# Performance work log

Measured on AMD Instinct MI355X. Metric: run time of the kernel, lower is better.

## Reference

```python
import jax, jax.numpy as jnp
import numpy as np

NP_, NA, NPR = 3000, 25, 1071
N = NP_ + NA + NPR          # 4096 total nodes
D = 256                     # latent_dim
H = 8                       # num_heads
DH = D // H                 # head dim 32
FF = 4 * D                  # feed-forward dim
BLOCKS = 3                  # args.block_num
E = 131072                  # edges = N * 32 avg degree
EPS = 1e-5


def setup_inputs() -> dict:
    key = jax.random.key(0)
    ks = jax.random.split(key, 16)
    s = 1.0 / np.sqrt(D)
    return {
        "adj_row": jax.random.randint(ks[0], (E,), 0, N, dtype=jnp.int32),
        "adj_col": jax.random.randint(ks[1], (E,), 0, N, dtype=jnp.int32),
        "adj_val": jax.random.uniform(ks[2], (E,), dtype=jnp.float32),
        "pe": jax.random.normal(ks[3], (NP_, D), dtype=jnp.float32) * s,
        "ae": jax.random.normal(ks[4], (NA, D), dtype=jnp.float32) * s,
        "qe": jax.random.normal(ks[5], (NPR, D), dtype=jnp.float32) * s,
        "Wqkv": jax.random.normal(ks[6], (D, 3 * D), dtype=jnp.float32) * s,
        "Wo": jax.random.normal(ks[7], (D, D), dtype=jnp.float32) * s,
        "W1": jax.random.normal(ks[8], (D, FF), dtype=jnp.float32) * s,
        "b1": jnp.zeros((FF,), dtype=jnp.float32),
        "W2": jax.random.normal(ks[9], (FF, D), dtype=jnp.float32) * (1.0 / np.sqrt(FF)),
        "b2": jnp.zeros((D,), dtype=jnp.float32),
        "ln1_g": jnp.ones((D,), dtype=jnp.float32),
        "ln1_b": jnp.zeros((D,), dtype=jnp.float32),
        "ln2_g": jnp.ones((D,), dtype=jnp.float32),
        "ln2_b": jnp.zeros((D,), dtype=jnp.float32),
    }


def _layer_norm(x, g, b):
    m = jnp.mean(x, axis=-1, keepdims=True)
    v = jnp.mean(jnp.square(x - m), axis=-1, keepdims=True)
    return (x - m) * jax.lax.rsqrt(v + EPS) * g + b


def _encoder_layer(x, Wqkv, Wo, W1, b1, W2, b2, ln1_g, ln1_b, ln2_g, ln2_b):
    # x: [N, D]; standard post-LN transformer encoder (dropout = 0)
    qkv = x @ Wqkv                                   # [N, 3D]
    q, k, v = jnp.split(qkv, 3, axis=-1)
    q = q.reshape(N, H, DH)
    k = k.reshape(N, H, DH)
    v = v.reshape(N, H, DH)
    scores = jnp.einsum("nhd,mhd->hnm", q, k) / np.sqrt(DH)  # [H, N, N]
    att = jax.nn.softmax(scores, axis=-1)
    o = jnp.einsum("hnm,mhd->nhd", att, v).reshape(N, D) @ Wo
    x = _layer_norm(x + o, ln1_g, ln1_b)
    h = jax.nn.relu(x @ W1 + b1) @ W2 + b2
    return _layer_norm(x + h, ln2_g, ln2_b)


def _spmm(adj_row, adj_col, adj_val, x):
    # sparse [N,N] @ dense [N,D] via gather + segment-sum scatter
    msgs = adj_val[:, None] * x[adj_col]             # [E, D]
    return jax.ops.segment_sum(msgs, adj_row, num_segments=N)


def reference(adj_row, adj_col, adj_val, pe, ae, qe, Wqkv, Wo, W1, b1, W2, b2,
              ln1_g, ln1_b, ln2_g, ln2_b):
    cur = jnp.concatenate([pe, ae, qe], axis=0)      # [N, D]
    total = cur
    for _ in range(BLOCKS):
        t = _spmm(adj_row, adj_col, adj_val, cur)
        t = _encoder_layer(t, Wqkv, Wo, W1, b1, W2, b2, ln1_g, ln1_b, ln2_g, ln2_b)
        cur = t + cur                                # residual per block
        total = total + cur                          # sum over embeds list
    protein = total[:NP_]
    aa = total[NP_:NP_ + NA]
    prop = total[NP_ + NA:]
    return total, protein, aa, prop
```

## Files before the change

### kernel.cpp

```cpp
#include <hip/hip_runtime.h>
#include <hip/hip_bf16.h>


#define NPROT 3000
#define NAA   25
#define NPROP 1071
#define NTOT  4096
#define DIM   256
#define NH    8
#define DHD   32
#define FFD   1024
#define NEDGE 131072
#define LNEPS 1e-5f
#define KSPLIT 2
#define KVQ (NTOT/KSPLIT)

typedef unsigned short u16;
typedef unsigned int u32;
typedef __attribute__((ext_vector_type(8))) short short8v;
typedef __attribute__((ext_vector_type(4))) float float4v;
typedef __attribute__((ext_vector_type(2))) unsigned int uint2v;

__device__ __forceinline__ u16 f2bu(float x){
  union { __hip_bfloat16 h; u16 u; } c; c.h = __float2bfloat16(x); return c.u;
}
__device__ __forceinline__ float bu2f(u16 u){
  union { u32 i; float f; } c; c.i = ((u32)u) << 16; return c.f;
}
__device__ __forceinline__ float4v mfma16(short8v a, short8v b, float4v c){
  return __builtin_amdgcn_mfma_f32_16x16x32_bf16(a, b, c, 0, 0, 0);
}
__device__ __forceinline__ u32 packbf(float lo, float hi){
  u32 ul = __builtin_bit_cast(u32, lo);
  u32 uh = __builtin_bit_cast(u32, hi);
  return (ul >> 16) | (uh & 0xFFFF0000u);
}

__global__ __launch_bounds__(256) void k_embed(const float* __restrict__ pe, const float* __restrict__ ae,
                                               const float* __restrict__ qe,
                                               float* __restrict__ cur, float* __restrict__ tot){
  int i = blockIdx.x*256 + threadIdx.x;
  int row = i >> 8;
  float v;
  if (row < NPROT)           v = pe[i];
  else if (row < NPROT+NAA)  v = ae[i - NPROT*DIM];
  else                       v = qe[i - (NPROT+NAA)*DIM];
  cur[i] = v; tot[i] = v;
}

__global__ __launch_bounds__(256) void k_zero(int* __restrict__ p, int n){
  int i = blockIdx.x*256 + threadIdx.x; if (i < n) p[i] = 0;
}

__global__ __launch_bounds__(256) void k_wconv_all(const float* __restrict__ Wqkv, const float* __restrict__ Wo,
                                                   const float* __restrict__ W1, const float* __restrict__ W2,
                                                   u16* __restrict__ wqkvt, u16* __restrict__ wot,
                                                   u16* __restrict__ w1t, u16* __restrict__ w2t){
  int b = blockIdx.x;
  const float* W; u16* Wt; int K, N, n;
  if (b < 768)       { W = Wqkv; Wt = wqkvt; K = 256;  N = 768;  n = b; }
  else if (b < 1024) { W = Wo;   Wt = wot;   K = 256;  N = 256;  n = b - 768; }
  else if (b < 2048) { W = W1;   Wt = w1t;   K = 256;  N = 1024; n = b - 1024; }
  else               { W = W2;   Wt = w2t;   K = 1024; N = 256;  n = b - 2048; }
  for (int k = threadIdx.x; k < K; k += 256)
    Wt[(size_t)n*K + k] = f2bu(W[(size_t)k*N + n]);
}

__global__ __launch_bounds__(256) void k_hist(const int* __restrict__ rows, int* __restrict__ cnt){
  int e = blockIdx.x*256 + threadIdx.x; if (e < NEDGE) atomicAdd(&cnt[rows[e]], 1);
}

__global__ __launch_bounds__(64) void k_scan(const int* __restrict__ cnt, int* __restrict__ rowptr,
                                             int* __restrict__ cursor){
  int lane = threadIdx.x;
  int sum = 0;
  for (int i = 0; i < 64; ++i) sum += cnt[lane*64 + i];
  int pref = sum;
  #pragma unroll
  for (int off = 1; off < 64; off <<= 1){
    int u = __shfl_up(pref, off);
    if (lane >= off) pref += u;
  }
  int run = pref - sum;
  for (int i = 0; i < 64; ++i){
    int c = cnt[lane*64 + i];
    rowptr[lane*64 + i] = run;
    cursor[lane*64 + i] = run;
    run += c;
  }
  if (lane == 63) rowptr[NTOT] = run;
}

__global__ __launch_bounds__(256) void k_scatter(const int* __restrict__ rows, const int* __restrict__ cols,
                                                 const float* __restrict__ vals, int* __restrict__ cursor,
                                                 int* __restrict__ ccol, float* __restrict__ cval){
  int e = blockIdx.x*256 + threadIdx.x; if (e >= NEDGE) return;
  int p = atomicAdd(&cursor[rows[e]], 1);
  ccol[p] = cols[e]; cval[p] = vals[e];
}

__global__ __launch_bounds__(256) void k_spmm(const int* __restrict__ rowptr, const int* __restrict__ ccol,
                                              const float* __restrict__ cval, const float* __restrict__ x,
                                              float* __restrict__ out, u16* __restrict__ outb){
  int r = blockIdx.x, c = threadIdx.x;
  int s = rowptr[r], e = rowptr[r+1];
  float acc = 0.f;
  for (int i = s; i < e; ++i)
    acc += cval[i] * x[((size_t)ccol[i] << 8) + c];
  out[((size_t)r << 8) + c] = acc;
  outb[((size_t)r << 8) + c] = f2bu(acc);
}

template<int RELU, int BIAS, int BF16OUT>
__global__ __launch_bounds__(256) void k_gemm64(const u16* __restrict__ A, const u16* __restrict__ Wt,
                                                const float* __restrict__ bias, void* __restrict__ Cv,
                                                int M, int K, int Nc){
  __shared__ u16 Al[64*64];
  __shared__ u16 Bl[64*64];
  const int tid = threadIdx.x;
  const int w  = tid >> 6, l = tid & 63, lr = l & 15, g = l >> 4;
  const int row0 = blockIdx.y*64, col0 = blockIdx.x*64;
  const int wm = (w >> 1)*32, wn = (w & 1)*32;
  const int sm = tid >> 2;
  const int so = (tid & 3)*2;
  float4v acc[2][2] = {};

  for (int k0 = 0; k0 < K; k0 += 64){
    const u16* As = A  + (size_t)(row0 + sm)*K + k0 + so*8;
    const u16* Bs = Wt + (size_t)(col0 + sm)*K + k0 + so*8;
    #pragma unroll
    for (int j = 0; j < 2; ++j){
      int o = so + j;
      int slot = o ^ (sm & 7);
      *(short8v*)(Al + sm*64 + slot*8) = *(const short8v*)(As + j*8);
      *(short8v*)(Bl + sm*64 + slot*8) = *(const short8v*)(Bs + j*8);
    }
    __syncthreads();
    #pragma unroll
    for (int kk = 0; kk < 2; ++kk){
      short8v af[2], bfr[2];
      #pragma unroll
      for (int i = 0; i < 2; ++i){
        int am = wm + 16*i + lr;
        af[i]  = *(const short8v*)(Al + am*64 + (((4*kk + g) ^ (am & 7))*8));
        int bn = wn + 16*i + lr;
        bfr[i] = *(const short8v*)(Bl + bn*64 + (((4*kk + g) ^ (bn & 7))*8));
      }
      acc[0][0] = mfma16(af[0], bfr[0], acc[0][0]);
      acc[0][1] = mfma16(af[0], bfr[1], acc[0][1]);
      acc[1][0] = mfma16(af[1], bfr[0], acc[1][0]);
      acc[1][1] = mfma16(af[1], bfr[1], acc[1][1]);
    }
    __syncthreads();
  }

  #pragma unroll
  for (int mi = 0; mi < 2; ++mi){
    #pragma unroll
    for (int ni = 0; ni < 2; ++ni){
      int col = col0 + wn + 16*ni + lr;
      float bv = BIAS ? bias[col] : 0.f;
      #pragma unroll
      for (int j = 0; j < 4; ++j){
        int row = row0 + wm + 16*mi + 4*g + j;
        float v = acc[mi][ni][j] + bv;
        if (RELU) v = fmaxf(v, 0.f);
        if (BF16OUT) ((u16*)Cv)[(size_t)row*Nc + col] = f2bu(v);
        else         ((float*)Cv)[(size_t)row*Nc + col] = v;
      }
    }
  }
}

__global__ __launch_bounds__(256) void k_attn_mfma(const u16* __restrict__ qbf,
                                                   u16* __restrict__ op,
                                                   float* __restrict__ mbuf, float* __restrict__ lbuf){
  __shared__ u16 Vt[2][32*64];
  __shared__ u16 Pl[4][16*64];
  __shared__ float Fl[4][16];
  const int h   = blockIdx.y;
  const int ks  = blockIdx.z;
  const int qb  = blockIdx.x * 64;
  const int tid = threadIdx.x;
  const int w   = tid >> 6;
  const int l   = tid & 63;
  const int lr  = l & 15;
  const int g   = l >> 4;
  const int sr  = tid >> 2;
  const int sq  = tid & 3;
  const float SC  = 0.17677669529663687f;
  const float SCL = 0.25503837f;
  const float DEFER = 31.368f;
  u16* opart = op + (size_t)ks*NTOT*DIM;

  short8v qf = *(const short8v*)(qbf + (size_t)(qb + 16*w + lr)*768 + h*DHD + 8*g);
  short8v ones;
  #pragma unroll
  for (int j = 0; j < 8; ++j) ones[j] = (short)0x3F80;

  float4v oa0 = {0.f,0.f,0.f,0.f}, oa1 = {0.f,0.f,0.f,0.f};
  float4v accl = {0.f,0.f,0.f,0.f};
  float mrun = -1e30f;
  u16* pw = &Pl[w][0];

  const u16* vp = qbf + (size_t)(ks*KVQ + sr)*768 + 512 + h*DHD + 8*sq;
  const u16* kp = qbf + (size_t)(ks*KVQ + lr)*768 + 256 + h*DHD + 8*g;
  short8v vreg = *(const short8v*)vp;
  short8v kf0 = *(const short8v*)(kp);
  short8v kf1 = *(const short8v*)(kp + (size_t)16*768);
  short8v kf2 = *(const short8v*)(kp + (size_t)32*768);
  short8v kf3 = *(const short8v*)(kp + (size_t)48*768);

  const int NIT = KVQ/64;
  for (int t = 0; t < NIT; ++t){
    u16* vt = &Vt[t & 1][0];
    #pragma unroll
    for (int j = 0; j < 8; ++j){
      int row  = 8*sq + j;
      int slot = (sr >> 3) ^ j;
      vt[row*64 + slot*8 + (sr & 7)] = (u16)vreg[j];
    }
    __syncthreads();
    vp += (size_t)64*768;
    if (t + 1 < NIT) vreg = *(const short8v*)vp;

    float4v s0 = mfma16(kf0, qf, (float4v){0.f,0.f,0.f,0.f});
    float4v s1 = mfma16(kf1, qf, (float4v){0.f,0.f,0.f,0.f});
    float4v s2 = mfma16(kf2, qf, (float4v){0.f,0.f,0.f,0.f});
    float4v s3 = mfma16(kf3, qf, (float4v){0.f,0.f,0.f,0.f});
    if (t + 1 < NIT){
      const u16* kn = kp + (size_t)(t+1)*64*768;
      kf0 = *(const short8v*)(kn);
      kf1 = *(const short8v*)(kn + (size_t)16*768);
      kf2 = *(const short8v*)(kn + (size_t)32*768);
      kf3 = *(const short8v*)(kn + (size_t)48*768);
    }

    float m0 = fmaxf(fmaxf(fmaxf(s0[0],s0[1]),s0[2]),s0[3]);
    float m1 = fmaxf(fmaxf(fmaxf(s1[0],s1[1]),s1[2]),s1[3]);
    float m2 = fmaxf(fmaxf(fmaxf(s2[0],s2[1]),s2[2]),s2[3]);
    float m3 = fmaxf(fmaxf(fmaxf(s3[0],s3[1]),s3[2]),s3[3]);
    float tm = fmaxf(fmaxf(fmaxf(m0,m1),m2),m3);
    tm = fmaxf(tm, __shfl_xor(tm, 16));
    tm = fmaxf(tm, __shfl_xor(tm, 32));
    const bool nomax = __all(tm <= mrun + DEFER);
    float fac = 1.f;
    if (!nomax){
      float mn = fmaxf(mrun, tm);
      fac = exp2f((mrun - mn)*SCL);
      mrun = mn;
    }
    float mns = mrun*SCL;
    #pragma unroll
    for (int j = 0; j < 4; ++j){
      s0[j] = exp2f(__builtin_fmaf(s0[j], SCL, -mns));
      s1[j] = exp2f(__builtin_fmaf(s1[j], SCL, -mns));
      s2[j] = exp2f(__builtin_fmaf(s2[j], SCL, -mns));
      s3[j] = exp2f(__builtin_fmaf(s3[j], SCL, -mns));
    }

    {
      int gh = g >> 1, gl = 4*(g & 1);
      uint2v* d0 = (uint2v*)(pw + lr*64 + ((0 + gh) ^ (lr & 7))*8 + gl);
      uint2v* d1 = (uint2v*)(pw + lr*64 + ((2 + gh) ^ (lr & 7))*8 + gl);
      uint2v* d2 = (uint2v*)(pw + lr*64 + ((4 + gh) ^ (lr & 7))*8 + gl);
      uint2v* d3 = (uint2v*)(pw + lr*64 + ((6 + gh) ^ (lr & 7))*8 + gl);
      *d0 = (uint2v){packbf(s0[0],s0[1]), packbf(s0[2],s0[3])};
      *d1 = (uint2v){packbf(s1[0],s1[1]), packbf(s1[2],s1[3])};
      *d2 = (uint2v){packbf(s2[0],s2[1]), packbf(s2[2],s2[3])};
      *d3 = (uint2v){packbf(s3[0],s3[1]), packbf(s3[2],s3[3])};
    }

    if (!nomax){
      if (g == 0) Fl[w][lr] = fac;
      float fq0 = Fl[w][4*g+0], fq1 = Fl[w][4*g+1], fq2 = Fl[w][4*g+2], fq3 = Fl[w][4*g+3];
      oa0[0]*=fq0; oa0[1]*=fq1; oa0[2]*=fq2; oa0[3]*=fq3;
      oa1[0]*=fq0; oa1[1]*=fq1; oa1[2]*=fq2; oa1[3]*=fq3;
      accl[0]*=fq0; accl[1]*=fq1; accl[2]*=fq2; accl[3]*=fq3;
    }

    #pragma unroll
    for (int kk = 0; kk < 2; ++kk){
      int slotp = (4*kk + g) ^ (lr & 7);
      short8v pa = *(const short8v*)(pw + lr*64 + slotp*8);
      short8v v0 = *(const short8v*)(vt + lr*64        + slotp*8);
      short8v v1 = *(const short8v*)(vt + (lr+16)*64   + slotp*8);
      oa0  = mfma16(pa, v0, oa0);
      oa1  = mfma16(pa, v1, oa1);
      accl = mfma16(pa, ones, accl);
    }
  }

  #pragma unroll
  for (int j = 0; j < 4; ++j){
    size_t row = (size_t)(qb + 16*w + 4*g + j);
    opart[row*DIM + h*DHD + lr]      = f2bu(oa0[j]);
    opart[row*DIM + h*DHD + 16 + lr] = f2bu(oa1[j]);
  }
  if (l < 16){
    size_t mi = (size_t)(ks*NH + h)*NTOT + qb + 16*w + lr;
    mbuf[mi] = mrun*SC;
  }
  if (lr == 0){
    #pragma unroll
    for (int j = 0; j < 4; ++j){
      size_t mi = (size_t)(ks*NH + h)*NTOT + qb + 16*w + 4*g + j;
      lbuf[mi] = accl[j];
    }
  }
}

__global__ __launch_bounds__(256) void k_attn_merge(const u16* __restrict__ op,
                                                    const float* __restrict__ mbuf, const float* __restrict__ lbuf,
                                                    u16* __restrict__ obf){
  int i = blockIdx.x*256 + threadIdx.x;
  int r = i >> 8, c = i & 255, h = c >> 5;
  float m[KSPLIT], wgt[KSPLIT];
  float M = -1e30f;
  #pragma unroll
  for (int k = 0; k < KSPLIT; ++k){
    m[k] = mbuf[(size_t)(k*NH + h)*NTOT + r];
    M = fmaxf(M, m[k]);
  }
  float L = 0.f, acc = 0.f;
  #pragma unroll
  for (int k = 0; k < KSPLIT; ++k){
    wgt[k] = __expf(m[k] - M);
    L   += wgt[k]*lbuf[(size_t)(k*NH + h)*NTOT + r];
    acc += wgt[k]*bu2f(op[(size_t)k*NTOT*DIM + i]);
  }
  obf[i] = f2bu(acc / L);
}

template<int DUAL>
__global__ __launch_bounds__(256) void k_add_ln(const float* __restrict__ a, const float* __restrict__ b,
                                                const float* __restrict__ g, const float* __restrict__ be,
                                                float* __restrict__ out, u16* __restrict__ out2){
  __shared__ float red[4];
  int r = blockIdx.x, c = threadIdx.x;
  float v = a[((size_t)r << 8) + c] + b[((size_t)r << 8) + c];
  float s = v;
  #pragma unroll
  for (int off = 32; off; off >>= 1) s += __shfl_down(s, off);
  if ((c & 63) == 0) red[c >> 6] = s;
  __syncthreads();
  float mean = (red[0]+red[1]+red[2]+red[3]) * (1.f/DIM);
  __syncthreads();
  float d = v - mean;
  float s2 = d*d;
  #pragma unroll
  for (int off = 32; off; off >>= 1) s2 += __shfl_down(s2, off);
  if ((c & 63) == 0) red[c >> 6] = s2;
  __syncthreads();
  float var = (red[0]+red[1]+red[2]+red[3]) * (1.f/DIM);
  float rv = d * rsqrtf(var + LNEPS) * g[c] + be[c];
  out[((size_t)r << 8) + c] = rv;
  if (DUAL) out2[((size_t)r << 8) + c] = f2bu(rv);
}

template<int FINAL>
__global__ __launch_bounds__(256) void k_add_ln_upd(const float* __restrict__ a, const float* __restrict__ b,
                                                    const float* __restrict__ g, const float* __restrict__ be,
                                                    float* __restrict__ cur, float* __restrict__ tot,
                                                    float* __restrict__ out){
  __shared__ float red[4];
  int r = blockIdx.x, c = threadIdx.x;
  size_t idx = ((size_t)r << 8) + c;
  float v = a[idx] + b[idx];
  float s = v;
  #pragma unroll
  for (int off = 32; off; off >>= 1) s += __shfl_down(s, off);
  if ((c & 63) == 0) red[c >> 6] = s;
  __syncthreads();
  float mean = (red[0]+red[1]+red[2]+red[3]) * (1.f/DIM);
  __syncthreads();
  float d = v - mean;
  float s2 = d*d;
  #pragma unroll
  for (int off = 32; off; off >>= 1) s2 += __shfl_down(s2, off);
  if ((c & 63) == 0) red[c >> 6] = s2;
  __syncthreads();
  float var = (red[0]+red[1]+red[2]+red[3]) * (1.f/DIM);
  float rv = d * rsqrtf(var + LNEPS) * g[c] + be[c];
  float cu = cur[idx] + rv;
  cur[idx] = cu;
  float tv = tot[idx] + cu;
  tot[idx] = tv;
  if (FINAL){
    out[idx] = tv;
    out[(size_t)NTOT*DIM + idx] = tv;
  }
}

extern "C" void kernel_launch(void* const* d_in, const int* in_sizes, int n_in,
                              void* d_out, int out_size, void* d_ws, size_t ws_size,
                              hipStream_t stream){
  const int*   adj_row = (const int*)  d_in[0];
  const int*   adj_col = (const int*)  d_in[1];
  const float* adj_val = (const float*)d_in[2];
  const float* pe   = (const float*)d_in[3];
  const float* ae   = (const float*)d_in[4];
  const float* qe   = (const float*)d_in[5];
  const float* Wqkv = (const float*)d_in[6];
  const float* Wo   = (const float*)d_in[7];
  const float* W1   = (const float*)d_in[8];
  const float* b1   = (const float*)d_in[9];
  const float* W2   = (const float*)d_in[10];
  const float* b2   = (const float*)d_in[11];
  const float* g1   = (const float*)d_in[12];
  const float* be1  = (const float*)d_in[13];
  const float* g2   = (const float*)d_in[14];
  const float* be2  = (const float*)d_in[15];
  float* out = (float*)d_out;

  char* w = (char*)d_ws;
  float* cur  = (float*)w; w += (size_t)NTOT*DIM*4;
  float* tot  = (float*)w; w += (size_t)NTOT*DIM*4;
  float* tf   = (float*)w; w += (size_t)NTOT*DIM*4;
  float* pbuf = (float*)w; w += (size_t)NTOT*DIM*4;
  float* x1   = (float*)w; w += (size_t)NTOT*DIM*4;
  u16* tbf    = (u16*)w;   w += (size_t)NTOT*DIM*2;
  u16* obf    = (u16*)w;   w += (size_t)NTOT*DIM*2;
  u16* x1b    = (u16*)w;   w += (size_t)NTOT*DIM*2;
  u16* hq     = (u16*)w;   w += (size_t)NTOT*FFD*2;
  u16* wqkvt  = (u16*)w;   w += (size_t)768*256*2;
  u16* wot    = (u16*)w;   w += (size_t)256*256*2;
  u16* w1t    = (u16*)w;   w += (size_t)1024*256*2;
  u16* w2t    = (u16*)w;   w += (size_t)256*1024*2;
  int* rowptr = (int*)w;   w += (size_t)(NTOT+1)*4;
  int* cnt    = (int*)w;   w += (size_t)NTOT*4;
  int* cursor = (int*)w;   w += (size_t)NTOT*4;
  int* ccol   = (int*)w;   w += (size_t)NEDGE*4;
  float* cval = (float*)w; w += (size_t)NEDGE*4;
  u16* qbf  = hq;
  u16* opbf = (u16*)pbuf;
  float* mbuf = (float*)tbf;
  float* lbuf = mbuf + (size_t)KSPLIT*NH*NTOT;

  k_zero<<<16, 256, 0, stream>>>(cnt, NTOT);
  k_embed<<<NTOT, 256, 0, stream>>>(pe, ae, qe, cur, tot);
  k_hist<<<NEDGE/256, 256, 0, stream>>>(adj_row, cnt);
  k_scan<<<1, 64, 0, stream>>>(cnt, rowptr, cursor);
  k_scatter<<<NEDGE/256, 256, 0, stream>>>(adj_row, adj_col, adj_val, cursor, ccol, cval);
  k_wconv_all<<<2304, 256, 0, stream>>>(Wqkv, Wo, W1, W2, wqkvt, wot, w1t, w2t);

  for (int blk = 0; blk < 3; ++blk){
    k_spmm<<<NTOT, 256, 0, stream>>>(rowptr, ccol, cval, cur, tf, tbf);
    k_gemm64<0,0,1><<<dim3(768/64, NTOT/64), 256, 0, stream>>>(tbf, wqkvt, nullptr, qbf, NTOT, 256, 768);
    k_attn_mfma<<<dim3(NTOT/64, NH, KSPLIT), 256, 0, stream>>>(qbf, opbf, mbuf, lbuf);
    k_attn_merge<<<NTOT*DIM/256, 256, 0, stream>>>(opbf, mbuf, lbuf, obf);
    k_gemm64<0,0,0><<<dim3(256/64, NTOT/64), 256, 0, stream>>>(obf, wot, nullptr, pbuf, NTOT, 256, 256);
    k_add_ln<1><<<NTOT, 256, 0, stream>>>(tf, pbuf, g1, be1, x1, x1b);
    k_gemm64<1,1,1><<<dim3(1024/64, NTOT/64), 256, 0, stream>>>(x1b, w1t, b1, hq, NTOT, 256, 1024);
    k_gemm64<0,1,0><<<dim3(256/64, NTOT/64), 256, 0, stream>>>(hq, w2t, b2, pbuf, NTOT, 1024, 256);
    if (blk < 2)
      k_add_ln_upd<0><<<NTOT, 256, 0, stream>>>(x1, pbuf, g2, be2, cur, tot, nullptr);
    else
      k_add_ln_upd<1><<<NTOT, 256, 0, stream>>>(x1, pbuf, g2, be2, cur, tot, out);
  }
}
```

Measured before the change: 476.1 us.

## Write V transposed from QKV GEMM and drop LDS V transpose in attention

```diff
diff --git a/kernel.cpp b/kernel.cpp
--- a/kernel.cpp
+++ b/kernel.cpp
@@ -111,9 +111,10 @@
   outb[((size_t)r << 8) + c] = f2bu(acc);
 }
 
-template<int RELU, int BIAS, int BF16OUT>
+template<int RELU, int BIAS, int BF16OUT, int VSPLIT>
 __global__ __launch_bounds__(256) void k_gemm64(const u16* __restrict__ A, const u16* __restrict__ Wt,
                                                 const float* __restrict__ bias, void* __restrict__ Cv,
+                                                u16* __restrict__ vtg,
                                                 int M, int K, int Nc){
   __shared__ u16 Al[64*64];
   __shared__ u16 Bl[64*64];
@@ -158,26 +159,33 @@
   for (int mi = 0; mi < 2; ++mi){
     #pragma unroll
     for (int ni = 0; ni < 2; ++ni){
-      int col = col0 + wn + 16*ni + lr;
-      float bv = BIAS ? bias[col] : 0.f;
-      #pragma unroll
-      for (int j = 0; j < 4; ++j){
-        int row = row0 + wm + 16*mi + 4*g + j;
-        float v = acc[mi][ni][j] + bv;
-        if (RELU) v = fmaxf(v, 0.f);
-        if (BF16OUT) ((u16*)Cv)[(size_t)row*Nc + col] = f2bu(v);
-        else         ((float*)Cv)[(size_t)row*Nc + col] = v;
+      int colbase = col0 + wn + 16*ni;
+      int col = colbase + lr;
+      if (VSPLIT && colbase >= 512){
+        int row = row0 + wm + 16*mi + 4*g;
+        u32 lo = packbf(acc[mi][ni][0], acc[mi][ni][1]);
+        u32 hi = packbf(acc[mi][ni][2], acc[mi][ni][3]);
+        *(uint2v*)(vtg + (size_t)(col - 512)*NTOT + row) = (uint2v){lo, hi};
+      } else {
+        float bv = BIAS ? bias[col] : 0.f;
+        #pragma unroll
+        for (int j = 0; j < 4; ++j){
+          int row = row0 + wm + 16*mi + 4*g + j;
+          float v = acc[mi][ni][j] + bv;
+          if (RELU) v = fmaxf(v, 0.f);
+          if (BF16OUT) ((u16*)Cv)[(size_t)row*Nc + col] = f2bu(v);
+          else         ((float*)Cv)[(size_t)row*Nc + col] = v;
+        }
       }
     }
   }
 }
 
 __global__ __launch_bounds__(256) void k_attn_mfma(const u16* __restrict__ qbf,
+                                                   const u16* __restrict__ vtg,
                                                    u16* __restrict__ op,
                                                    float* __restrict__ mbuf, float* __restrict__ lbuf){
-  __shared__ u16 Vt[2][32*64];
   __shared__ u16 Pl[4][16*64];
-  __shared__ float Fl[4][16];
   const int h   = blockIdx.y;
   const int ks  = blockIdx.z;
   const int qb  = blockIdx.x * 64;
@@ -186,8 +194,6 @@
   const int l   = tid & 63;
   const int lr  = l & 15;
   const int g   = l >> 4;
-  const int sr  = tid >> 2;
-  const int sq  = tid & 3;
   const float SC  = 0.17677669529663687f;
   const float SCL = 0.25503837f;
   const float DEFER = 31.368f;
@@ -203,9 +209,9 @@
   float mrun = -1e30f;
   u16* pw = &Pl[w][0];
 
-  const u16* vp = qbf + (size_t)(ks*KVQ + sr)*768 + 512 + h*DHD + 8*sq;
   const u16* kp = qbf + (size_t)(ks*KVQ + lr)*768 + 256 + h*DHD + 8*g;
-  short8v vreg = *(const short8v*)vp;
+  const u16* vr0 = vtg + (size_t)(h*DHD + lr)*NTOT + ks*KVQ + 8*g;
+  const u16* vr1 = vr0 + (size_t)16*NTOT;
   short8v kf0 = *(const short8v*)(kp);
   short8v kf1 = *(const short8v*)(kp + (size_t)16*768);
   short8v kf2 = *(const short8v*)(kp + (size_t)32*768);
@@ -213,28 +219,15 @@
 
   const int NIT = KVQ/64;
   for (int t = 0; t < NIT; ++t){
-    u16* vt = &Vt[t & 1][0];
-    #pragma unroll
-    for (int j = 0; j < 8; ++j){
-      int row  = 8*sq + j;
-      int slot = (sr >> 3) ^ j;
-      vt[row*64 + slot*8 + (sr & 7)] = (u16)vreg[j];
-    }
-    __syncthreads();
-    vp += (size_t)64*768;
-    if (t + 1 < NIT) vreg = *(const short8v*)vp;
-
     float4v s0 = mfma16(kf0, qf, (float4v){0.f,0.f,0.f,0.f});
     float4v s1 = mfma16(kf1, qf, (float4v){0.f,0.f,0.f,0.f});
     float4v s2 = mfma16(kf2, qf, (float4v){0.f,0.f,0.f,0.f});
     float4v s3 = mfma16(kf3, qf, (float4v){0.f,0.f,0.f,0.f});
-    if (t + 1 < NIT){
-      const u16* kn = kp + (size_t)(t+1)*64*768;
-      kf0 = *(const short8v*)(kn);
-      kf1 = *(const short8v*)(kn + (size_t)16*768);
-      kf2 = *(const short8v*)(kn + (size_t)32*768);
-      kf3 = *(const short8v*)(kn + (size_t)48*768);
-    }
+    kp += (size_t)64*768;
+    kf0 = *(const short8v*)(kp);
+    kf1 = *(const short8v*)(kp + (size_t)16*768);
+    kf2 = *(const short8v*)(kp + (size_t)32*768);
+    kf3 = *(const short8v*)(kp + (size_t)48*768);
 
     float m0 = fmaxf(fmaxf(fmaxf(s0[0],s0[1]),s0[2]),s0[3]);
     float m1 = fmaxf(fmaxf(fmaxf(s1[0],s1[1]),s1[2]),s1[3]);
@@ -272,41 +265,36 @@
     }
 
     if (!nomax){
-      if (g == 0) Fl[w][lr] = fac;
-      float fq0 = Fl[w][4*g+0], fq1 = Fl[w][4*g+1], fq2 = Fl[w][4*g+2], fq3 = Fl[w][4*g+3];
-      oa0[0]*=fq0; oa0[1]*=fq1; oa0[2]*=fq2; oa0[3]*=fq3;
-      oa1[0]*=fq0; oa1[1]*=fq1; oa1[2]*=fq2; oa1[3]*=fq3;
-      accl[0]*=fq0; accl[1]*=fq1; accl[2]*=fq2; accl[3]*=fq3;
-    }
-
+      oa0[0]*=fac; oa0[1]*=fac; oa0[2]*=fac; oa0[3]*=fac;
+      oa1[0]*=fac; oa1[1]*=fac; oa1[2]*=fac; oa1[3]*=fac;
+      accl[0]*=fac; accl[1]*=fac; accl[2]*=fac; accl[3]*=fac;
+    }
+
+    const u16* vb = vr0 + (size_t)t*64;
+    const u16* vb1 = vr1 + (size_t)t*64;
     #pragma unroll
     for (int kk = 0; kk < 2; ++kk){
       int slotp = (4*kk + g) ^ (lr & 7);
       short8v pa = *(const short8v*)(pw + lr*64 + slotp*8);
-      short8v v0 = *(const short8v*)(vt + lr*64        + slotp*8);
-      short8v v1 = *(const short8v*)(vt + (lr+16)*64   + slotp*8);
-      oa0  = mfma16(pa, v0, oa0);
-      oa1  = mfma16(pa, v1, oa1);
-      accl = mfma16(pa, ones, accl);
-    }
-  }
-
-  #pragma unroll
-  for (int j = 0; j < 4; ++j){
-    size_t row = (size_t)(qb + 16*w + 4*g + j);
-    opart[row*DIM + h*DHD + lr]      = f2bu(oa0[j]);
-    opart[row*DIM + h*DHD + 16 + lr] = f2bu(oa1[j]);
-  }
-  if (l < 16){
+      short8v va0 = *(const short8v*)(vb  + 32*kk);
+      short8v va1 = *(const short8v*)(vb1 + 32*kk);
+      oa0  = mfma16(va0, pa, oa0);
+      oa1  = mfma16(va1, pa, oa1);
+      accl = mfma16(ones, pa, accl);
+    }
+  }
+
+  {
+    size_t row = (size_t)(qb + 16*w + lr);
+    u32 a0 = packbf(oa0[0], oa0[1]), a1 = packbf(oa0[2], oa0[3]);
+    u32 b0 = packbf(oa1[0], oa1[1]), b1 = packbf(oa1[2], oa1[3]);
+    *(uint2v*)(opart + row*DIM + h*DHD + 4*g)      = (uint2v){a0, a1};
+    *(uint2v*)(opart + row*DIM + h*DHD + 16 + 4*g) = (uint2v){b0, b1};
+  }
+  if (g == 0){
     size_t mi = (size_t)(ks*NH + h)*NTOT + qb + 16*w + lr;
     mbuf[mi] = mrun*SC;
-  }
-  if (lr == 0){
-    #pragma unroll
-    for (int j = 0; j < 4; ++j){
-      size_t mi = (size_t)(ks*NH + h)*NTOT + qb + 16*w + 4*g + j;
-      lbuf[mi] = accl[j];
-    }
+    lbuf[mi] = accl[0];
   }
 }
 
@@ -433,6 +421,7 @@
   int* ccol   = (int*)w;   w += (size_t)NEDGE*4;
   float* cval = (float*)w; w += (size_t)NEDGE*4;
   u16* qbf  = hq;
+  u16* vtg  = obf;
   u16* opbf = (u16*)pbuf;
   float* mbuf = (float*)tbf;
   float* lbuf = mbuf + (size_t)KSPLIT*NH*NTOT;
@@ -446,13 +435,13 @@
 
   for (int blk = 0; blk < 3; ++blk){
     k_spmm<<<NTOT, 256, 0, stream>>>(rowptr, ccol, cval, cur, tf, tbf);
-    k_gemm64<0,0,1><<<dim3(768/64, NTOT/64), 256, 0, stream>>>(tbf, wqkvt, nullptr, qbf, NTOT, 256, 768);
-    k_attn_mfma<<<dim3(NTOT/64, NH, KSPLIT), 256, 0, stream>>>(qbf, opbf, mbuf, lbuf);
+    k_gemm64<0,0,1,1><<<dim3(768/64, NTOT/64), 256, 0, stream>>>(tbf, wqkvt, nullptr, qbf, vtg, NTOT, 256, 768);
+    k_attn_mfma<<<dim3(NTOT/64, NH, KSPLIT), 256, 0, stream>>>(qbf, vtg, opbf, mbuf, lbuf);
     k_attn_merge<<<NTOT*DIM/256, 256, 0, stream>>>(opbf, mbuf, lbuf, obf);
-    k_gemm64<0,0,0><<<dim3(256/64, NTOT/64), 256, 0, stream>>>(obf, wot, nullptr, pbuf, NTOT, 256, 256);
+    k_gemm64<0,0,0,0><<<dim3(256/64, NTOT/64), 256, 0, stream>>>(obf, wot, nullptr, pbuf, nullptr, NTOT, 256, 256);
     k_add_ln<1><<<NTOT, 256, 0, stream>>>(tf, pbuf, g1, be1, x1, x1b);
-    k_gemm64<1,1,1><<<dim3(1024/64, NTOT/64), 256, 0, stream>>>(x1b, w1t, b1, hq, NTOT, 256, 1024);
-    k_gemm64<0,1,0><<<dim3(256/64, NTOT/64), 256, 0, stream>>>(hq, w2t, b2, pbuf, NTOT, 1024, 256);
+    k_gemm64<1,1,1,0><<<dim3(1024/64, NTOT/64), 256, 0, stream>>>(x1b, w1t, b1, hq, nullptr, NTOT, 256, 1024);
+    k_gemm64<0,1,0,0><<<dim3(256/64, NTOT/64), 256, 0, stream>>>(hq, w2t, b2, pbuf, nullptr, NTOT, 1024, 256);
     if (blk < 2)
       k_add_ln_upd<0><<<NTOT, 256, 0, stream>>>(x1, pbuf, g2, be2, cur, tot, nullptr);
     else
```

Result: slower. 627.8 us (+31.8%).
